# Optimization experiments

Measured on AMD Instinct MI355X. Metric: run time of the kernel, lower is better.

Reference implementation:

```python
import jax, jax.numpy as jnp
import numpy as np

N_NODES = 10000
N_EDGES = 320000
D = 128  # feature dim for edges, nodes, globals


def setup_inputs() -> dict:
    key = jax.random.key(0)
    ks = jax.random.split(key, 8)
    edges = jax.random.normal(ks[0], (N_EDGES, D), dtype=jnp.float32)
    nodes = jax.random.normal(ks[1], (N_NODES, D), dtype=jnp.float32)
    globals_ = jax.random.normal(ks[2], (D,), dtype=jnp.float32)
    receivers = jax.random.randint(ks[3], (N_EDGES,), 0, N_NODES, dtype=jnp.int32).astype(jnp.int64)
    senders = jax.random.randint(ks[4], (N_EDGES,), 0, N_NODES, dtype=jnp.int32).astype(jnp.int64)
    W1 = jax.random.normal(ks[5], (4 * D, 256), dtype=jnp.float32) * (1.0 / np.sqrt(4 * D))
    b1 = jnp.zeros((256,), dtype=jnp.float32)
    W2 = jax.random.normal(ks[6], (256, D), dtype=jnp.float32) * (1.0 / np.sqrt(256))
    b2 = jnp.zeros((D,), dtype=jnp.float32)
    return {"edges": edges, "nodes": nodes, "globals_": globals_,
            "receivers": receivers, "senders": senders,
            "W1": W1, "b1": b1, "W2": W2, "b2": b2}


def reference(edges, nodes, globals_, receivers, senders, W1, b1, W2, b2):
    # Gather adjacent node features to edges, broadcast globals, concat.
    recv_feats = nodes[receivers]                 # [E, D]
    send_feats = nodes[senders]                   # [E, D]
    glob_feats = jnp.broadcast_to(globals_, (edges.shape[0], globals_.shape[0]))  # [E, D]
    x = jnp.concatenate([edges, recv_feats, send_feats, glob_feats], axis=-1)     # [E, 4D]
    # Edge-update MLP: 4D -> 256 -> D with relu.
    h = jax.nn.relu(x @ W1 + b1)
    new_edges = h @ W2 + b2                       # [E, D]
    return new_edges
```

## Files before the change

kernel.cpp:

```cpp
#include <hip/hip_runtime.h>
#include <hip/hip_bf16.h>

#define D 128
#define NH 256
#define K1 384
#define BM 64
#define E_TOTAL 320000
#define NNODES 10000

typedef __attribute__((ext_vector_type(8))) short bf16x8;
typedef __attribute__((ext_vector_type(4))) float f32x4;

__device__ __forceinline__ unsigned short f2b(float f) {
  unsigned int u = __builtin_bit_cast(unsigned int, f);
  u += 0x7fffu + ((u >> 16) & 1u);
  return (unsigned short)(u >> 16);
}

__global__ void cast_nodes_kernel(const float* __restrict__ nodes,
                                  ushort* __restrict__ out) {
  int i = (blockIdx.x * 256 + threadIdx.x) * 4;
  float4 v = *(const float4*)(nodes + i);
  ushort4 b;
  b.x = f2b(v.x); b.y = f2b(v.y); b.z = f2b(v.z); b.w = f2b(v.w);
  *(ushort4*)(out + i) = b;
}

__global__ void pack_w1_kernel(const float* __restrict__ W1,
                               ushort* __restrict__ W1p) {
  int c = blockIdx.x * 256 + threadIdx.x;
  int nt = c / (12 * 64);
  int rem = c % (12 * 64);
  int ks = rem >> 6;
  int l = rem & 63;
  int col = nt * 16 + (l & 15);
  int k0 = ks * 32 + (l >> 4) * 8;
  ushort* dst = W1p + (size_t)c * 8;
  #pragma unroll
  for (int j = 0; j < 8; ++j)
    dst[j] = f2b(W1[(size_t)(k0 + j) * NH + col]);
}

__global__ void pack_w2_kernel(const float* __restrict__ W2,
                               ushort* __restrict__ W2p) {
  int c = blockIdx.x * 256 + threadIdx.x;
  int nt2 = c / (8 * 64);
  int rem = c % (8 * 64);
  int ks = rem >> 6;
  int l = rem & 63;
  int col = nt2 * 16 + (l & 15);
  int k0 = ks * 32 + (l >> 4) * 8;
  ushort* dst = W2p + (size_t)c * 8;
  #pragma unroll
  for (int j = 0; j < 8; ++j)
    dst[j] = f2b(W2[(size_t)(k0 + j) * D + col]);
}

__global__ void cvec_kernel(const float* __restrict__ W1,
                            const float* __restrict__ b1,
                            const float* __restrict__ g,
                            float* __restrict__ cvec) {
  int n = threadIdx.x;
  float acc = b1[n];
  for (int k = 0; k < D; ++k)
    acc += g[k] * W1[(size_t)(K1 + k) * NH + n];
  cvec[n] = acc;
}

__global__ __launch_bounds__(512, 4) void fused_kernel(
    const float* __restrict__ edges,
    const ushort* __restrict__ nodes_b,
    const int* __restrict__ receivers,
    const int* __restrict__ senders,
    const ushort* __restrict__ W1p,
    const float* __restrict__ cvec,
    const ushort* __restrict__ W2p,
    const float* __restrict__ b2,
    float* __restrict__ out) {
  __shared__ char Xs[BM * 768];
  __shared__ char Hs[BM * 512];

  const int ebase = blockIdx.x * BM;
  const int tid = threadIdx.x;

  const int gr0 = tid >> 4;
  const int gr1 = gr0 + 32;
  const int gc = (tid & 15) << 3;
  int idx_r0 = receivers[ebase + gr0];
  int idx_r1 = receivers[ebase + gr1];
  int idx_s0 = senders[ebase + gr0];
  int idx_s1 = senders[ebase + gr1];

  float4 ev[4];
  int er[4], ec[4];
  #pragma unroll
  for (int it = 0; it < 4; ++it) {
    int ch = tid + it * 512;
    er[it] = ch >> 5;
    ec[it] = (ch & 31) << 2;
    ev[it] = *(const float4*)(edges + (size_t)(ebase + er[it]) * D + ec[it]);
  }

  uint4 gv[4];
  gv[0] = *(const uint4*)(nodes_b + (size_t)idx_r0 * D + gc);
  gv[1] = *(const uint4*)(nodes_b + (size_t)idx_r1 * D + gc);
  gv[2] = *(const uint4*)(nodes_b + (size_t)idx_s0 * D + gc);
  gv[3] = *(const uint4*)(nodes_b + (size_t)idx_s1 * D + gc);

  #pragma unroll
  for (int it = 0; it < 4; ++it) {
    ushort4 b;
    b.x = f2b(ev[it].x); b.y = f2b(ev[it].y); b.z = f2b(ev[it].z); b.w = f2b(ev[it].w);
    *(ushort4*)(Xs + er[it] * 768 + ((ec[it] * 2) ^ ((er[it] & 7) << 4))) = b;
  }
  {
    int cR = (D + gc) * 2, cS = (2 * D + gc) * 2;
    *(uint4*)(Xs + gr0 * 768 + (cR ^ ((gr0 & 7) << 4))) = gv[0];
    *(uint4*)(Xs + gr1 * 768 + (cR ^ ((gr1 & 7) << 4))) = gv[1];
    *(uint4*)(Xs + gr0 * 768 + (cS ^ ((gr0 & 7) << 4))) = gv[2];
    *(uint4*)(Xs + gr1 * 768 + (cS ^ ((gr1 & 7) << 4))) = gv[3];
  }
  __syncthreads();

  const int lane = tid & 63;
  const int wave = tid >> 6;
  const int lr = lane & 15;
  const int kg = lane >> 4;

  float cv[2];
  #pragma unroll
  for (int n = 0; n < 2; ++n) cv[n] = cvec[wave * 32 + n * 16 + lr];
  float bias2 = b2[wave * 16 + lr];

  const ushort* w1base = W1p + (size_t)(wave * 2) * 12 * 512 + lane * 8;

  f32x4 acc[4][2] = {};
  bf16x8 bb[2][2];
  #pragma unroll
  for (int n = 0; n < 2; ++n)
    bb[0][n] = *(const bf16x8*)(w1base + (size_t)n * 12 * 512);

  #pragma unroll
  for (int ks = 0; ks < 12; ++ks) {
    const int cur = ks & 1, nxt = cur ^ 1;
    if (ks < 11) {
      #pragma unroll
      for (int n = 0; n < 2; ++n)
        bb[nxt][n] = *(const bf16x8*)(w1base + (size_t)n * 12 * 512 + (ks + 1) * 512);
    }
    const int k0 = ks * 32 + kg * 8;
    bf16x8 a[4];
    #pragma unroll
    for (int m = 0; m < 4; ++m) {
      int row = m * 16 + lr;
      a[m] = *(const bf16x8*)(Xs + row * 768 + ((k0 * 2) ^ ((row & 7) << 4)));
    }
    #pragma unroll
    for (int m = 0; m < 4; ++m)
      #pragma unroll
      for (int n = 0; n < 2; ++n)
        acc[m][n] = __builtin_amdgcn_mfma_f32_16x16x32_bf16(a[m], bb[cur][n], acc[m][n], 0, 0, 0);
  }

  #pragma unroll
  for (int n = 0; n < 2; ++n) {
    int col = wave * 32 + n * 16 + lr;
    #pragma unroll
    for (int m = 0; m < 4; ++m) {
      #pragma unroll
      for (int r = 0; r < 4; ++r) {
        int row = m * 16 + kg * 4 + r;
        float v = acc[m][n][r] + cv[n];
        v = v > 0.f ? v : 0.f;
        *(ushort*)(Hs + row * 512 + ((col * 2) ^ ((row & 7) << 4))) = f2b(v);
      }
    }
  }

  const ushort* w2base = W2p + (size_t)wave * 8 * 512 + lane * 8;
  bf16x8 b2b[2];
  b2b[0] = *(const bf16x8*)(w2base);
  __syncthreads();

  f32x4 acc2[4] = {};
  #pragma unroll
  for (int ks = 0; ks < 8; ++ks) {
    const int cur = ks & 1, nxt = cur ^ 1;
    if (ks < 7)
      b2b[nxt] = *(const bf16x8*)(w2base + (ks + 1) * 512);
    const int k0 = ks * 32 + kg * 8;
    bf16x8 a[4];
    #pragma unroll
    for (int m = 0; m < 4; ++m) {
      int row = m * 16 + lr;
      a[m] = *(const bf16x8*)(Hs + row * 512 + ((k0 * 2) ^ ((row & 7) << 4)));
    }
    #pragma unroll
    for (int m = 0; m < 4; ++m)
      acc2[m] = __builtin_amdgcn_mfma_f32_16x16x32_bf16(a[m], b2b[cur], acc2[m], 0, 0, 0);
  }

  {
    int col = wave * 16 + lr;
    #pragma unroll
    for (int m = 0; m < 4; ++m) {
      #pragma unroll
      for (int r = 0; r < 4; ++r) {
        int row = m * 16 + kg * 4 + r;
        out[(size_t)(ebase + row) * D + col] = acc2[m][r] + bias2;
      }
    }
  }
}

extern "C" void kernel_launch(void* const* d_in, const int* in_sizes, int n_in,
                              void* d_out, int out_size, void* d_ws, size_t ws_size,
                              hipStream_t stream) {
  const float* edges     = (const float*)d_in[0];
  const float* nodes     = (const float*)d_in[1];
  const float* globals_  = (const float*)d_in[2];
  const int*   receivers = (const int*)d_in[3];
  const int*   senders   = (const int*)d_in[4];
  const float* W1        = (const float*)d_in[5];
  const float* b1        = (const float*)d_in[6];
  const float* W2        = (const float*)d_in[7];
  const float* b2        = (const float*)d_in[8];
  float* out = (float*)d_out;

  char* ws = (char*)d_ws;
  ushort* nodes_b = (ushort*)ws;
  ushort* W1p     = (ushort*)(ws + 2560000);
  ushort* W2p     = (ushort*)(ws + 2560000 + 196608);
  float*  cvec    = (float*)(ws + 2560000 + 196608 + 65536);

  hipLaunchKernelGGL(cast_nodes_kernel, dim3(NNODES * D / 1024), dim3(256), 0, stream,
                     nodes, nodes_b);
  hipLaunchKernelGGL(pack_w1_kernel, dim3(48), dim3(256), 0, stream, W1, W1p);
  hipLaunchKernelGGL(pack_w2_kernel, dim3(16), dim3(256), 0, stream, W2, W2p);
  hipLaunchKernelGGL(cvec_kernel, dim3(1), dim3(256), 0, stream,
                     W1, b1, globals_, cvec);
  hipLaunchKernelGGL(fused_kernel, dim3(E_TOTAL / BM), dim3(512), 0, stream,
                     edges, nodes_b, receivers, senders, W1p, cvec, W2p, b2, out);
}
```

Baseline: 144.7 us.

## Alias X and H shared buffers, retile second GEMM 2x2, add MFMA priority

The hidden-activation buffer now reuses the input-tile shared memory, with an extra barrier between the end of GEMM1 and the H writes. This cuts LDS per block from 80KB to 48KB, and launch bounds are raised to 6 blocks/CU. The second GEMM changes from 1x4 M tiles per wave to a 2x2 (M,N) wave tiling, which cuts redundant A-fragment LDS reads. s_setprio is placed around the MFMA bursts to favour matrix issue. Tighter launch bounds may force register spills, and the added barrier adds a sync point.

```diff
diff --git a/kernel.cpp b/kernel.cpp
--- a/kernel.cpp
+++ b/kernel.cpp
@@ -67,7 +67,7 @@
   cvec[n] = acc;
 }
 
-__global__ __launch_bounds__(512, 4) void fused_kernel(
+__global__ __launch_bounds__(512, 6) void fused_kernel(
     const float* __restrict__ edges,
     const ushort* __restrict__ nodes_b,
     const int* __restrict__ receivers,
@@ -77,8 +77,9 @@
     const ushort* __restrict__ W2p,
     const float* __restrict__ b2,
     float* __restrict__ out) {
-  __shared__ char Xs[BM * 768];
-  __shared__ char Hs[BM * 512];
+  __shared__ char Smem[BM * 768];
+  char* Xs = Smem;
+  char* Hs = Smem;
 
   const int ebase = blockIdx.x * BM;
   const int tid = threadIdx.x;
@@ -130,7 +131,11 @@
   float cv[2];
   #pragma unroll
   for (int n = 0; n < 2; ++n) cv[n] = cvec[wave * 32 + n * 16 + lr];
-  float bias2 = b2[wave * 16 + lr];
+  const int wm2 = wave >> 2;
+  const int wn2 = wave & 3;
+  float bias2[2];
+  #pragma unroll
+  for (int n = 0; n < 2; ++n) bias2[n] = b2[wn2 * 32 + n * 16 + lr];
 
   const ushort* w1base = W1p + (size_t)(wave * 2) * 12 * 512 + lane * 8;
 
@@ -155,12 +160,22 @@
       int row = m * 16 + lr;
       a[m] = *(const bf16x8*)(Xs + row * 768 + ((k0 * 2) ^ ((row & 7) << 4)));
     }
+    __builtin_amdgcn_s_setprio(1);
     #pragma unroll
     for (int m = 0; m < 4; ++m)
       #pragma unroll
       for (int n = 0; n < 2; ++n)
         acc[m][n] = __builtin_amdgcn_mfma_f32_16x16x32_bf16(a[m], bb[cur][n], acc[m][n], 0, 0, 0);
-  }
+    __builtin_amdgcn_s_setprio(0);
+  }
+
+  const ushort* w2base0 = W2p + (size_t)(wn2 * 2) * 8 * 512 + lane * 8;
+  bf16x8 b2b[2][2];
+  #pragma unroll
+  for (int n = 0; n < 2; ++n)
+    b2b[0][n] = *(const bf16x8*)(w2base0 + (size_t)n * 8 * 512);
+
+  __syncthreads();
 
   #pragma unroll
   for (int n = 0; n < 2; ++n) {
@@ -176,38 +191,42 @@
       }
     }
   }
-
-  const ushort* w2base = W2p + (size_t)wave * 8 * 512 + lane * 8;
-  bf16x8 b2b[2];
-  b2b[0] = *(const bf16x8*)(w2base);
   __syncthreads();
 
-  f32x4 acc2[4] = {};
+  f32x4 acc2[2][2] = {};
   #pragma unroll
   for (int ks = 0; ks < 8; ++ks) {
     const int cur = ks & 1, nxt = cur ^ 1;
-    if (ks < 7)
-      b2b[nxt] = *(const bf16x8*)(w2base + (ks + 1) * 512);
+    if (ks < 7) {
+      #pragma unroll
+      for (int n = 0; n < 2; ++n)
+        b2b[nxt][n] = *(const bf16x8*)(w2base0 + (size_t)n * 8 * 512 + (ks + 1) * 512);
+    }
     const int k0 = ks * 32 + kg * 8;
-    bf16x8 a[4];
-    #pragma unroll
-    for (int m = 0; m < 4; ++m) {
-      int row = m * 16 + lr;
+    bf16x8 a[2];
+    #pragma unroll
+    for (int m = 0; m < 2; ++m) {
+      int row = wm2 * 32 + m * 16 + lr;
       a[m] = *(const bf16x8*)(Hs + row * 512 + ((k0 * 2) ^ ((row & 7) << 4)));
     }
-    #pragma unroll
-    for (int m = 0; m < 4; ++m)
-      acc2[m] = __builtin_amdgcn_mfma_f32_16x16x32_bf16(a[m], b2b[cur], acc2[m], 0, 0, 0);
-  }
-
-  {
-    int col = wave * 16 + lr;
-    #pragma unroll
-    for (int m = 0; m < 4; ++m) {
+    __builtin_amdgcn_s_setprio(1);
+    #pragma unroll
+    for (int m = 0; m < 2; ++m)
+      #pragma unroll
+      for (int n = 0; n < 2; ++n)
+        acc2[m][n] = __builtin_amdgcn_mfma_f32_16x16x32_bf16(a[m], b2b[cur][n], acc2[m][n], 0, 0, 0);
+    __builtin_amdgcn_s_setprio(0);
+  }
+
+  #pragma unroll
+  for (int n = 0; n < 2; ++n) {
+    int col = wn2 * 32 + n * 16 + lr;
+    #pragma unroll
+    for (int m = 0; m < 2; ++m) {
       #pragma unroll
       for (int r = 0; r < 4; ++r) {
-        int row = m * 16 + kg * 4 + r;
-        out[(size_t)(ebase + row) * D + col] = acc2[m][r] + bias2;
+        int row = wm2 * 32 + m * 16 + kg * 4 + r;
+        out[(size_t)(ebase + row) * D + col] = acc2[m][n][r] + bias2[n];
       }
     }
   }
```

Measured after the change: 187.5 us. +29.6%, slower.

## Swap MFMA operand roles so outputs are transposed for vectorized stores

Applied to the files above, without the earlier changes.

Both GEMMs now pass the weight fragment as the A operand and the activations as B, so each lane's accumulator holds four consecutive feature columns for one edge. The hidden tile is written to LDS with packed 8-byte stores and the output with float4 stores, replacing scalar 2-byte and 4-byte scattered writes. The second GEMM is also retiled as a 4x2 wave grid of 32x32 tiles, so each wave loads two W2 fragments and reads two H fragments per k-step instead of one and four. This trades a different register layout and extra bias registers for fewer, wider memory transactions.

```diff
diff --git a/kernel.cpp b/kernel.cpp
--- a/kernel.cpp
+++ b/kernel.cpp
@@ -127,88 +127,115 @@
   const int lr = lane & 15;
   const int kg = lane >> 4;
 
-  float cv[2];
-  #pragma unroll
-  for (int n = 0; n < 2; ++n) cv[n] = cvec[wave * 32 + n * 16 + lr];
-  float bias2 = b2[wave * 16 + lr];
+  float cv_[2][4];
+  #pragma unroll
+  for (int ht = 0; ht < 2; ++ht)
+    #pragma unroll
+    for (int r = 0; r < 4; ++r)
+      cv_[ht][r] = cvec[wave * 32 + ht * 16 + kg * 4 + r];
+
+  const int wm3 = wave >> 1;
+  const int wn3 = wave & 1;
+  float bias_[2][4];
+  #pragma unroll
+  for (int mt = 0; mt < 2; ++mt)
+    #pragma unroll
+    for (int r = 0; r < 4; ++r)
+      bias_[mt][r] = b2[wm3 * 32 + mt * 16 + kg * 4 + r];
 
   const ushort* w1base = W1p + (size_t)(wave * 2) * 12 * 512 + lane * 8;
 
-  f32x4 acc[4][2] = {};
-  bf16x8 bb[2][2];
-  #pragma unroll
-  for (int n = 0; n < 2; ++n)
-    bb[0][n] = *(const bf16x8*)(w1base + (size_t)n * 12 * 512);
+  f32x4 acc[2][4] = {};
+  bf16x8 aw[2][2];
+  #pragma unroll
+  for (int ht = 0; ht < 2; ++ht)
+    aw[0][ht] = *(const bf16x8*)(w1base + (size_t)ht * 12 * 512);
 
   #pragma unroll
   for (int ks = 0; ks < 12; ++ks) {
     const int cur = ks & 1, nxt = cur ^ 1;
     if (ks < 11) {
       #pragma unroll
-      for (int n = 0; n < 2; ++n)
-        bb[nxt][n] = *(const bf16x8*)(w1base + (size_t)n * 12 * 512 + (ks + 1) * 512);
+      for (int ht = 0; ht < 2; ++ht)
+        aw[nxt][ht] = *(const bf16x8*)(w1base + (size_t)ht * 12 * 512 + (ks + 1) * 512);
     }
     const int k0 = ks * 32 + kg * 8;
-    bf16x8 a[4];
-    #pragma unroll
-    for (int m = 0; m < 4; ++m) {
-      int row = m * 16 + lr;
-      a[m] = *(const bf16x8*)(Xs + row * 768 + ((k0 * 2) ^ ((row & 7) << 4)));
-    }
-    #pragma unroll
-    for (int m = 0; m < 4; ++m)
-      #pragma unroll
-      for (int n = 0; n < 2; ++n)
-        acc[m][n] = __builtin_amdgcn_mfma_f32_16x16x32_bf16(a[m], bb[cur][n], acc[m][n], 0, 0, 0);
-  }
-
-  #pragma unroll
-  for (int n = 0; n < 2; ++n) {
-    int col = wave * 32 + n * 16 + lr;
-    #pragma unroll
-    for (int m = 0; m < 4; ++m) {
-      #pragma unroll
-      for (int r = 0; r < 4; ++r) {
-        int row = m * 16 + kg * 4 + r;
-        float v = acc[m][n][r] + cv[n];
-        v = v > 0.f ? v : 0.f;
-        *(ushort*)(Hs + row * 512 + ((col * 2) ^ ((row & 7) << 4))) = f2b(v);
-      }
-    }
-  }
-
-  const ushort* w2base = W2p + (size_t)wave * 8 * 512 + lane * 8;
-  bf16x8 b2b[2];
-  b2b[0] = *(const bf16x8*)(w2base);
+    bf16x8 xb[4];
+    #pragma unroll
+    for (int et = 0; et < 4; ++et) {
+      int row = et * 16 + lr;
+      xb[et] = *(const bf16x8*)(Xs + row * 768 + ((k0 * 2) ^ ((row & 7) << 4)));
+    }
+    #pragma unroll
+    for (int ht = 0; ht < 2; ++ht)
+      #pragma unroll
+      for (int et = 0; et < 4; ++et)
+        acc[ht][et] = __builtin_amdgcn_mfma_f32_16x16x32_bf16(aw[cur][ht], xb[et], acc[ht][et], 0, 0, 0);
+  }
+
+  #pragma unroll
+  for (int ht = 0; ht < 2; ++ht) {
+    const int h0b = (wave * 32 + ht * 16 + kg * 4) * 2;
+    #pragma unroll
+    for (int et = 0; et < 4; ++et) {
+      int e = et * 16 + lr;
+      float v0 = acc[ht][et][0] + cv_[ht][0];
+      float v1 = acc[ht][et][1] + cv_[ht][1];
+      float v2 = acc[ht][et][2] + cv_[ht][2];
+      float v3 = acc[ht][et][3] + cv_[ht][3];
+      v0 = v0 > 0.f ? v0 : 0.f;
+      v1 = v1 > 0.f ? v1 : 0.f;
+      v2 = v2 > 0.f ? v2 : 0.f;
+      v3 = v3 > 0.f ? v3 : 0.f;
+      uint2 pk;
+      pk.x = (unsigned)f2b(v0) | ((unsigned)f2b(v1) << 16);
+      pk.y = (unsigned)f2b(v2) | ((unsigned)f2b(v3) << 16);
+      *(uint2*)(Hs + e * 512 + (h0b ^ ((e & 7) << 4))) = pk;
+    }
+  }
+
+  const ushort* w2base = W2p + (size_t)(wm3 * 2) * 8 * 512 + lane * 8;
+  bf16x8 aw2[2][2];
+  #pragma unroll
+  for (int mt = 0; mt < 2; ++mt)
+    aw2[0][mt] = *(const bf16x8*)(w2base + (size_t)mt * 8 * 512);
   __syncthreads();
 
-  f32x4 acc2[4] = {};
+  f32x4 acc2[2][2] = {};
   #pragma unroll
   for (int ks = 0; ks < 8; ++ks) {
     const int cur = ks & 1, nxt = cur ^ 1;
-    if (ks < 7)
-      b2b[nxt] = *(const bf16x8*)(w2base + (ks + 1) * 512);
+    if (ks < 7) {
+      #pragma unroll
+      for (int mt = 0; mt < 2; ++mt)
+        aw2[nxt][mt] = *(const bf16x8*)(w2base + (size_t)mt * 8 * 512 + (ks + 1) * 512);
+    }
     const int k0 = ks * 32 + kg * 8;
-    bf16x8 a[4];
-    #pragma unroll
-    for (int m = 0; m < 4; ++m) {
-      int row = m * 16 + lr;
-      a[m] = *(const bf16x8*)(Hs + row * 512 + ((k0 * 2) ^ ((row & 7) << 4)));
-    }
-    #pragma unroll
-    for (int m = 0; m < 4; ++m)
-      acc2[m] = __builtin_amdgcn_mfma_f32_16x16x32_bf16(a[m], b2b[cur], acc2[m], 0, 0, 0);
-  }
-
-  {
-    int col = wave * 16 + lr;
-    #pragma unroll
-    for (int m = 0; m < 4; ++m) {
-      #pragma unroll
-      for (int r = 0; r < 4; ++r) {
-        int row = m * 16 + kg * 4 + r;
-        out[(size_t)(ebase + row) * D + col] = acc2[m][r] + bias2;
-      }
+    bf16x8 hb[2];
+    #pragma unroll
+    for (int et2 = 0; et2 < 2; ++et2) {
+      int e = wn3 * 32 + et2 * 16 + lr;
+      hb[et2] = *(const bf16x8*)(Hs + e * 512 + ((k0 * 2) ^ ((e & 7) << 4)));
+    }
+    #pragma unroll
+    for (int mt = 0; mt < 2; ++mt)
+      #pragma unroll
+      for (int et2 = 0; et2 < 2; ++et2)
+        acc2[mt][et2] = __builtin_amdgcn_mfma_f32_16x16x32_bf16(aw2[cur][mt], hb[et2], acc2[mt][et2], 0, 0, 0);
+  }
+
+  #pragma unroll
+  for (int mt = 0; mt < 2; ++mt) {
+    const int c0 = wm3 * 32 + mt * 16 + kg * 4;
+    #pragma unroll
+    for (int et2 = 0; et2 < 2; ++et2) {
+      int e = wn3 * 32 + et2 * 16 + lr;
+      float4 o;
+      o.x = acc2[mt][et2][0] + bias_[mt][0];
+      o.y = acc2[mt][et2][1] + bias_[mt][1];
+      o.z = acc2[mt][et2][2] + bias_[mt][2];
+      o.w = acc2[mt][et2][3] + bias_[mt][3];
+      *(float4*)(out + (size_t)(ebase + e) * D + c0) = o;
     }
   }
 }
```

Measured after the change: 156.6 us. 8.2% more time.

## Make fused edge MLP persistent with double-buffered async gather prefetch

Applied to the files above, without the earlier changes.

Replaces one-block-per-tile launch with 256 persistent blocks that loop over tiles. Each block double-buffers LDS for the edge and gathered node features. Node rows for the next tile are gathered with global_load_lds directly into shared memory, and next-tile edges and indices are prefetched into registers while the current tile's MFMA work runs. The aim is to hide gather and load latency behind compute. In exchange it uses more LDS, drops the occupancy hint from 4 to 2, and runs only 256 blocks, which may underfill the GPU.

```diff
diff --git a/kernel.cpp b/kernel.cpp
--- a/kernel.cpp
+++ b/kernel.cpp
@@ -5,7 +5,8 @@
 #define NH 256
 #define K1 384
 #define BM 64
-#define E_TOTAL 320000
+#define NTILES 5000
+#define NBLK 256
 #define NNODES 10000
 
 typedef __attribute__((ext_vector_type(8))) short bf16x8;
@@ -15,6 +16,20 @@
   unsigned int u = __builtin_bit_cast(unsigned int, f);
   u += 0x7fffu + ((u >> 16) & 1u);
   return (unsigned short)(u >> 16);
+}
+__device__ __forceinline__ unsigned pk2(float a, float b) {
+  return (unsigned)f2b(a) | ((unsigned)f2b(b) << 16);
+}
+__device__ __forceinline__ uint4 pack8(float4 a, float4 b) {
+  uint4 r;
+  r.x = pk2(a.x, a.y); r.y = pk2(a.z, a.w);
+  r.z = pk2(b.x, b.y); r.w = pk2(b.z, b.w);
+  return r;
+}
+__device__ __forceinline__ void gload16(const void* g, void* l) {
+  __builtin_amdgcn_global_load_lds(
+      (const __attribute__((address_space(1))) void*)g,
+      (__attribute__((address_space(3))) void*)l, 16, 0, 0);
 }
 
 __global__ void cast_nodes_kernel(const float* __restrict__ nodes,
@@ -67,7 +82,7 @@
   cvec[n] = acc;
 }
 
-__global__ __launch_bounds__(512, 4) void fused_kernel(
+__global__ __launch_bounds__(512, 2) void fused_kernel(
     const float* __restrict__ edges,
     const ushort* __restrict__ nodes_b,
     const int* __restrict__ receivers,
@@ -77,139 +92,179 @@
     const ushort* __restrict__ W2p,
     const float* __restrict__ b2,
     float* __restrict__ out) {
-  __shared__ char Xs[BM * 768];
+  __shared__ char Xe[2][BM * 256];
+  __shared__ char Xg[2][BM * 512];
   __shared__ char Hs[BM * 512];
 
-  const int ebase = blockIdx.x * BM;
   const int tid = threadIdx.x;
-
-  const int gr0 = tid >> 4;
-  const int gr1 = gr0 + 32;
-  const int gc = (tid & 15) << 3;
-  int idx_r0 = receivers[ebase + gr0];
-  int idx_r1 = receivers[ebase + gr1];
-  int idx_s0 = senders[ebase + gr0];
-  int idx_s1 = senders[ebase + gr1];
-
-  float4 ev[4];
-  int er[4], ec[4];
-  #pragma unroll
-  for (int it = 0; it < 4; ++it) {
-    int ch = tid + it * 512;
-    er[it] = ch >> 5;
-    ec[it] = (ch & 31) << 2;
-    ev[it] = *(const float4*)(edges + (size_t)(ebase + er[it]) * D + ec[it]);
-  }
-
-  uint4 gv[4];
-  gv[0] = *(const uint4*)(nodes_b + (size_t)idx_r0 * D + gc);
-  gv[1] = *(const uint4*)(nodes_b + (size_t)idx_r1 * D + gc);
-  gv[2] = *(const uint4*)(nodes_b + (size_t)idx_s0 * D + gc);
-  gv[3] = *(const uint4*)(nodes_b + (size_t)idx_s1 * D + gc);
-
-  #pragma unroll
-  for (int it = 0; it < 4; ++it) {
-    ushort4 b;
-    b.x = f2b(ev[it].x); b.y = f2b(ev[it].y); b.z = f2b(ev[it].z); b.w = f2b(ev[it].w);
-    *(ushort4*)(Xs + er[it] * 768 + ((ec[it] * 2) ^ ((er[it] & 7) << 4))) = b;
-  }
-  {
-    int cR = (D + gc) * 2, cS = (2 * D + gc) * 2;
-    *(uint4*)(Xs + gr0 * 768 + (cR ^ ((gr0 & 7) << 4))) = gv[0];
-    *(uint4*)(Xs + gr1 * 768 + (cR ^ ((gr1 & 7) << 4))) = gv[1];
-    *(uint4*)(Xs + gr0 * 768 + (cS ^ ((gr0 & 7) << 4))) = gv[2];
-    *(uint4*)(Xs + gr1 * 768 + (cS ^ ((gr1 & 7) << 4))) = gv[3];
-  }
-  __syncthreads();
-
   const int lane = tid & 63;
   const int wave = tid >> 6;
   const int lr = lane & 15;
   const int kg = lane >> 4;
 
+  const int l31 = lane & 31;
+  const int myr = wave * 8 + (lane >> 5);
+  const int gc2 = (l31 * 16) & 255;
+  const int gsec = (l31 >= 16);
+  const int* __restrict__ myarr = gsec ? senders : receivers;
+
+  const int erow0 = tid >> 4;
+  const int ecc = (tid & 15) * 16;
+
   float cv[2];
   #pragma unroll
   for (int n = 0; n < 2; ++n) cv[n] = cvec[wave * 32 + n * 16 + lr];
-  float bias2 = b2[wave * 16 + lr];
-
+  const float bias = b2[wave * 16 + lr];
   const ushort* w1base = W1p + (size_t)(wave * 2) * 12 * 512 + lane * 8;
-
-  f32x4 acc[4][2] = {};
-  bf16x8 bb[2][2];
-  #pragma unroll
-  for (int n = 0; n < 2; ++n)
-    bb[0][n] = *(const bf16x8*)(w1base + (size_t)n * 12 * 512);
-
-  #pragma unroll
-  for (int ks = 0; ks < 12; ++ks) {
-    const int cur = ks & 1, nxt = cur ^ 1;
-    if (ks < 11) {
-      #pragma unroll
-      for (int n = 0; n < 2; ++n)
-        bb[nxt][n] = *(const bf16x8*)(w1base + (size_t)n * 12 * 512 + (ks + 1) * 512);
-    }
-    const int k0 = ks * 32 + kg * 8;
-    bf16x8 a[4];
-    #pragma unroll
-    for (int m = 0; m < 4; ++m) {
-      int row = m * 16 + lr;
-      a[m] = *(const bf16x8*)(Xs + row * 768 + ((k0 * 2) ^ ((row & 7) << 4)));
-    }
-    #pragma unroll
-    for (int m = 0; m < 4; ++m)
-      #pragma unroll
-      for (int n = 0; n < 2; ++n)
-        acc[m][n] = __builtin_amdgcn_mfma_f32_16x16x32_bf16(a[m], bb[cur][n], acc[m][n], 0, 0, 0);
+  const ushort* w2base = W2p + (size_t)wave * 8 * 512 + lane * 8;
+
+  int t = blockIdx.x;
+  int idxn[4];
+
+  {
+    const int eb = t * BM;
+    int idx0[4];
+    #pragma unroll
+    for (int j = 0; j < 4; ++j) idx0[j] = myarr[eb + myr + 2 * j];
+    #pragma unroll
+    for (int j = 0; j < 4; ++j) {
+      int r = myr + 2 * j;
+      gload16(nodes_b + (size_t)idx0[j] * D + ((gc2 ^ ((r & 7) << 4)) >> 1),
+              &Xg[0][wave * 4096 + j * 1024]);
+    }
+    #pragma unroll
+    for (int q = 0; q < 2; ++q) {
+      int row = erow0 + q * 32;
+      const float* ep = edges + (size_t)(eb + row) * D + (ecc >> 1);
+      float4 u0 = *(const float4*)ep;
+      float4 u1 = *(const float4*)(ep + 4);
+      *(uint4*)(&Xe[0][row * 256 + (ecc ^ ((row & 7) << 4))]) = pack8(u0, u1);
+    }
+    const int tn0 = (t + NBLK < NTILES) ? t + NBLK : t;
+    #pragma unroll
+    for (int j = 0; j < 4; ++j) idxn[j] = myarr[tn0 * BM + myr + 2 * j];
+    __syncthreads();
   }
 
-  #pragma unroll
-  for (int n = 0; n < 2; ++n) {
-    int col = wave * 32 + n * 16 + lr;
-    #pragma unroll
-    for (int m = 0; m < 4; ++m) {
-      #pragma unroll
-      for (int r = 0; r < 4; ++r) {
-        int row = m * 16 + kg * 4 + r;
-        float v = acc[m][n][r] + cv[n];
-        v = v > 0.f ? v : 0.f;
-        *(ushort*)(Hs + row * 512 + ((col * 2) ^ ((row & 7) << 4))) = f2b(v);
-      }
-    }
-  }
-
-  const ushort* w2base = W2p + (size_t)wave * 8 * 512 + lane * 8;
-  bf16x8 b2b[2];
-  b2b[0] = *(const bf16x8*)(w2base);
-  __syncthreads();
-
-  f32x4 acc2[4] = {};
-  #pragma unroll
-  for (int ks = 0; ks < 8; ++ks) {
-    const int cur = ks & 1, nxt = cur ^ 1;
-    if (ks < 7)
-      b2b[nxt] = *(const bf16x8*)(w2base + (ks + 1) * 512);
-    const int k0 = ks * 32 + kg * 8;
-    bf16x8 a[4];
-    #pragma unroll
-    for (int m = 0; m < 4; ++m) {
-      int row = m * 16 + lr;
-      a[m] = *(const bf16x8*)(Hs + row * 512 + ((k0 * 2) ^ ((row & 7) << 4)));
-    }
-    #pragma unroll
-    for (int m = 0; m < 4; ++m)
-      acc2[m] = __builtin_amdgcn_mfma_f32_16x16x32_bf16(a[m], b2b[cur], acc2[m], 0, 0, 0);
-  }
-
-  {
-    int col = wave * 16 + lr;
-    #pragma unroll
-    for (int m = 0; m < 4; ++m) {
-      #pragma unroll
-      for (int r = 0; r < 4; ++r) {
-        int row = m * 16 + kg * 4 + r;
-        out[(size_t)(ebase + row) * D + col] = acc2[m][r] + bias2;
-      }
-    }
+  int cur = 0;
+  for (; t < NTILES; t += NBLK) {
+    const int eb = t * BM;
+    const int tn = (t + NBLK < NTILES) ? t + NBLK : t;
+    const int t2 = (t + 2 * NBLK < NTILES) ? t + 2 * NBLK : tn;
+    const int ebn = tn * BM, eb2 = t2 * BM;
+    const int nxt = cur ^ 1;
+
+    #pragma unroll
+    for (int j = 0; j < 4; ++j) {
+      int r = myr + 2 * j;
+      gload16(nodes_b + (size_t)idxn[j] * D + ((gc2 ^ ((r & 7) << 4)) >> 1),
+              &Xg[nxt][wave * 4096 + j * 1024]);
+    }
+    float4 ev[4];
+    #pragma unroll
+    for (int q = 0; q < 2; ++q) {
+      int row = erow0 + q * 32;
+      const float* ep = edges + (size_t)(ebn + row) * D + (ecc >> 1);
+      ev[2 * q]     = *(const float4*)ep;
+      ev[2 * q + 1] = *(const float4*)(ep + 4);
+    }
+    int idx2[4];
+    #pragma unroll
+    for (int j = 0; j < 4; ++j) idx2[j] = myarr[eb2 + myr + 2 * j];
+
+    f32x4 acc[4][2] = {};
+    bf16x8 bb[2][2];
+    #pragma unroll
+    for (int n = 0; n < 2; ++n)
+      bb[0][n] = *(const bf16x8*)(w1base + (size_t)n * 12 * 512);
+    #pragma unroll
+    for (int ks = 0; ks < 12; ++ks) {
+      const int c1 = ks & 1, nx1 = c1 ^ 1;
+      if (ks < 11) {
+        #pragma unroll
+        for (int n = 0; n < 2; ++n)
+          bb[nx1][n] = *(const bf16x8*)(w1base + (size_t)n * 12 * 512 + (ks + 1) * 512);
+      }
+      const int k0 = ks * 32 + kg * 8;
+      bf16x8 a[4];
+      #pragma unroll
+      for (int m = 0; m < 4; ++m) {
+        int row = m * 16 + lr;
+        int swz = (row & 7) << 4;
+        const char* ap;
+        if (ks < 4)       ap = &Xe[cur][row * 256 + ((k0 * 2) ^ swz)];
+        else if (ks < 8)  ap = &Xg[cur][row * 512 + (((k0 - 128) * 2) ^ swz)];
+        else              ap = &Xg[cur][row * 512 + 256 + (((k0 - 256) * 2) ^ swz)];
+        a[m] = *(const bf16x8*)ap;
+      }
+      #pragma unroll
+      for (int m = 0; m < 4; ++m)
+        #pragma unroll
+        for (int n = 0; n < 2; ++n)
+          acc[m][n] = __builtin_amdgcn_mfma_f32_16x16x32_bf16(a[m], bb[c1][n], acc[m][n], 0, 0, 0);
+    }
+
+    bf16x8 b2b[2];
+    b2b[0] = *(const bf16x8*)w2base;
+
+    #pragma unroll
+    for (int n = 0; n < 2; ++n) {
+      int col = wave * 32 + n * 16 + lr;
+      #pragma unroll
+      for (int m = 0; m < 4; ++m) {
+        #pragma unroll
+        for (int r = 0; r < 4; ++r) {
+          int row = m * 16 + kg * 4 + r;
+          float v = acc[m][n][r] + cv[n];
+          v = v > 0.f ? v : 0.f;
+          *(ushort*)(&Hs[row * 512 + ((col * 2) ^ ((row & 7) << 4))]) = f2b(v);
+        }
+      }
+    }
+
+    __syncthreads();
+
+    f32x4 acc2[4] = {};
+    #pragma unroll
+    for (int ks = 0; ks < 8; ++ks) {
+      const int c2 = ks & 1, nx2 = c2 ^ 1;
+      if (ks < 7)
+        b2b[nx2] = *(const bf16x8*)(w2base + (ks + 1) * 512);
+      const int k0 = ks * 32 + kg * 8;
+      bf16x8 a2[4];
+      #pragma unroll
+      for (int m = 0; m < 4; ++m) {
+        int row = m * 16 + lr;
+        a2[m] = *(const bf16x8*)(&Hs[row * 512 + ((k0 * 2) ^ ((row & 7) << 4))]);
+      }
+      #pragma unroll
+      for (int m = 0; m < 4; ++m)
+        acc2[m] = __builtin_amdgcn_mfma_f32_16x16x32_bf16(a2[m], b2b[c2], acc2[m], 0, 0, 0);
+    }
+    {
+      int col = wave * 16 + lr;
+      #pragma unroll
+      for (int m = 0; m < 4; ++m) {
+        #pragma unroll
+        for (int r = 0; r < 4; ++r) {
+          int row = m * 16 + kg * 4 + r;
+          out[(size_t)(eb + row) * D + col] = acc2[m][r] + bias;
+        }
+      }
+    }
+
+    #pragma unroll
+    for (int q = 0; q < 2; ++q) {
+      int row = erow0 + q * 32;
+      *(uint4*)(&Xe[nxt][row * 256 + (ecc ^ ((row & 7) << 4))]) =
+          pack8(ev[2 * q], ev[2 * q + 1]);
+    }
+
+    #pragma unroll
+    for (int j = 0; j < 4; ++j) idxn[j] = idx2[j];
+
+    __syncthreads();
+    cur = nxt;
   }
 }
 
@@ -239,6 +294,6 @@
   hipLaunchKernelGGL(pack_w2_kernel, dim3(16), dim3(256), 0, stream, W2, W2p);
   hipLaunchKernelGGL(cvec_kernel, dim3(1), dim3(256), 0, stream,
                      W1, b1, globals_, cvec);
-  hipLaunchKernelGGL(fused_kernel, dim3(E_TOTAL / BM), dim3(512), 0, stream,
+  hipLaunchKernelGGL(fused_kernel, dim3(NBLK), dim3(512), 0, stream,
                      edges, nodes_b, receivers, senders, W1p, cvec, W2p, b2, out);
 }
```

Result: faster. 133.6 us (-7.6%).
